# Kernel optimization log

Measured on AMD Instinct MI355X. Metric: run time of the kernel, lower is better.

## Reference

```python
import jax, jax.numpy as jnp
import numpy as np

V_SIZE, E, H = 30000, 256, 128   # vocab, emb_dim, GRU hidden per direction
B, U, T, ND = 32, 32, 128, 64    # dialogues, utterances, max tokens, dialogue-id table size
SCALE = E ** 0.5                  # attention normalise_factor = hid_size**0.5, hid_size = emb_dim


def _gru_dir(x_seq, w_ih, w_hh, b_ih, b_hh):
    """Unidirectional torch-style GRU. x_seq: [N,T,E] -> [N,T,H]."""
    xp = jnp.einsum('nte,ge->ntg', x_seq, w_ih) + b_ih   # precompute input gates [N,T,3H]
    xp = jnp.swapaxes(xp, 0, 1)                          # [T,N,3H]

    def step(h, xpt):
        gh = h @ w_hh.T + b_hh
        r = jax.nn.sigmoid(xpt[:, :H] + gh[:, :H])
        z = jax.nn.sigmoid(xpt[:, H:2 * H] + gh[:, H:2 * H])
        n = jnp.tanh(xpt[:, 2 * H:] + r * gh[:, 2 * H:])
        h_new = (1.0 - z) * n + z * h
        return h_new, h_new

    h0 = jnp.zeros((x_seq.shape[0], H), x_seq.dtype)
    _, out = jax.lax.scan(step, h0, xp)
    return jnp.swapaxes(out, 0, 1)


def _forward(x, d_ids, utt_len, emb_table,
             w_ih_f, w_hh_f, b_ih_f, b_hh_f,
             w_ih_b, w_hh_b, b_ih_b, b_hh_b,
             wq, bq, wk, bk, wv, bv, wo, bo, wl, bl):
    b, u, t = x.shape
    N = b * u
    emb = emb_table[x.reshape(N, t)]                      # [N,T,E]
    lens = jnp.clip(utt_len[d_ids].reshape(N), 1, t)      # valid tokens per utterance
    pos = jnp.arange(t)
    # index map that reverses the valid prefix (padding region clipped, unused)
    rev_idx = jnp.clip(lens[:, None] - 1 - pos[None, :], 0, t - 1)  # [N,T]

    o_f = _gru_dir(emb, w_ih_f, w_hh_f, b_ih_f, b_hh_f)   # causal => correct on valid prefix
    emb_rev = jnp.take_along_axis(emb, rev_idx[:, :, None], axis=1)
    o_b = jnp.take_along_axis(_gru_dir(emb_rev, w_ih_b, w_hh_b, b_ih_b, b_hh_b),
                              rev_idx[:, :, None], axis=1)
    h = jnp.concatenate([o_f, o_b], axis=-1)              # [N,T,E] bi-GRU states

    # self-attention pooling; original takes op[-1], so only the query at the
    # last valid token (lens-1) is needed -- identical math, less compute.
    k = jnp.einsum('nte,he->nth', h, wk) + bk
    v = jnp.einsum('nte,he->nth', h, wv) + bv
    h_last = jnp.take_along_axis(h, (lens - 1)[:, None, None], axis=1)[:, 0]  # [N,E]
    q = h_last @ wq.T + bq
    score = jnp.einsum('nh,nth->nt', q, k) / SCALE
    score = jnp.where(pos[None, :] < lens[:, None], score, -jnp.inf)
    attn = jax.nn.softmax(score, axis=-1)
    ctx = jnp.einsum('nt,nth->nh', attn, v)
    out = (ctx @ wo.T + bo) @ wl.T + bl                   # make_output then final linear
    return out.reshape(b, u, -1)


def setup_inputs() -> dict:
    key = jax.random.key(0)
    ks = jax.random.split(key, 16)

    def p(k, shape):
        return (jax.random.normal(k, shape, jnp.float32) / np.sqrt(shape[-1])).astype(jnp.float32)

    return {
        'x': jax.random.randint(ks[0], (B, U, T), 0, V_SIZE, dtype=jnp.int32),
        'd_ids': jax.random.randint(ks[1], (B,), 0, ND, dtype=jnp.int32),
        'utt_len': jax.random.randint(ks[2], (ND, U), 1, T + 1, dtype=jnp.int32),
        'emb_table': p(ks[3], (V_SIZE, E)),
        'w_ih_f': p(ks[4], (3 * H, E)), 'w_hh_f': p(ks[5], (3 * H, H)),
        'b_ih_f': jnp.zeros(3 * H, jnp.float32), 'b_hh_f': jnp.zeros(3 * H, jnp.float32),
        'w_ih_b': p(ks[6], (3 * H, E)), 'w_hh_b': p(ks[7], (3 * H, H)),
        'b_ih_b': jnp.zeros(3 * H, jnp.float32), 'b_hh_b': jnp.zeros(3 * H, jnp.float32),
        'wq': p(ks[8], (E, E)), 'bq': jnp.zeros(E, jnp.float32),
        'wk': p(ks[9], (E, E)), 'bk': jnp.zeros(E, jnp.float32),
        'wv': p(ks[10], (E, E)), 'bv': jnp.zeros(E, jnp.float32),
        'wo': p(ks[11], (E, E)), 'bo': jnp.zeros(E, jnp.float32),
        'wl': p(ks[12], (E, E)), 'bl': jnp.zeros(E, jnp.float32),
    }


def reference(x, d_ids, utt_len, emb_table,
              w_ih_f, w_hh_f, b_ih_f, b_hh_f,
              w_ih_b, w_hh_b, b_ih_b, b_hh_b,
              wq, bq, wk, bk, wv, bv, wo, bo, wl, bl):
    return _forward(x, d_ids, utt_len, emb_table,
                    w_ih_f, w_hh_f, b_ih_f, b_hh_f,
                    w_ih_b, w_hh_b, b_ih_b, b_hh_b,
                    wq, bq, wk, bk, wv, bv, wo, bo, wl, bl)
```

## Files before the change

kernel.cpp:

```cpp
#include <hip/hip_runtime.h>
#include <hip/hip_bf16.h>
#include <math.h>
#include <stdint.h>

typedef unsigned short u16;
typedef unsigned int   u32;
typedef __attribute__((ext_vector_type(8))) short bf16x8;
typedef __attribute__((ext_vector_type(4))) float f32x4;

#define EDIM 256
#define HDIM 128
#define TLEN 128
#define NUTT 1024
#define UU   32
#define NBU  8

#define WS_FLAG 0
#define WS_LENS 64
#define WS_TAB  4608
#define WS_COPY 8192
#define WS_OF   18874368LL
#define WS_OB   52428800LL

#define MFMA16(a, b, c) __builtin_amdgcn_mfma_f32_16x16x32_bf16((a), (b), (c), 0, 0, 0)
#define SOUT(u, s, j) ((u) * 1096 + (s) * 136 + (j))
#define IS_TILED(a) ((a)==9||(a)==11||(a)==12||(a)==14||(a)==16)

__constant__ int G_SZ[18] = {7680000, 98304, 49152, 384, 384, 98304, 49152, 384, 384,
                             65536, 256, 65536, 65536, 256, 65536, 256, 65536, 256};

__device__ __forceinline__ float b2f(u16 b) {
    u32 u = ((u32)b) << 16; float f; __builtin_memcpy(&f, &u, 4); return f;
}
__device__ __forceinline__ u16 f2b(float f) {
    u32 u; __builtin_memcpy(&u, &f, 4);
    u32 r = u + 0x7FFFu + ((u >> 16) & 1u);
    return (u16)(r >> 16);
}
__device__ __forceinline__ u16 f2b_hw(float f) {
    __hip_bfloat16 h = __float2bfloat16(f);
    u16 v; __builtin_memcpy(&v, &h, 2); return v;
}
__device__ __forceinline__ float fsigmoid(float x) { return 1.0f / (1.0f + __expf(-x)); }
__device__ __forceinline__ float ftanh(float x) { return 1.0f - 2.0f / (__expf(2.0f * x) + 1.0f); }

__global__ __launch_bounds__(256)
void k_convert(void* ws,
               const int* __restrict__ d_ids, const int* __restrict__ utt_len,
               const void* a0, const void* a1, const void* a2, const void* a3,
               const void* a4, const void* a5, const void* a6, const void* a7,
               const void* a8, const void* a9, const void* a10, const void* a11,
               const void* a12, const void* a13, const void* a14, const void* a15,
               const void* a16, const void* a17) {
    __shared__ int scnt[4];
    const int tid = threadIdx.x, lane = tid & 63, wid = tid >> 6;
    const u16* p = (const u16*)a0;
    int cnt = 0;
#pragma unroll 8
    for (int i = tid; i < 16384; i += 256)
        cnt += ((p[i] & 0x7F80) == 0x7F80) ? 1 : 0;
#pragma unroll
    for (int o = 32; o > 0; o >>= 1) cnt += __shfl_down(cnt, o);
    if (lane == 0) scnt[wid] = cnt;
    __syncthreads();
    const int flag = (scnt[0] + scnt[1] + scnt[2] + scnt[3] > 0) ? 1 : 0;

    const void* orig[18] = {a0,a1,a2,a3,a4,a5,a6,a7,a8,a9,a10,a11,a12,a13,a14,a15,a16,a17};
    u16* base = (u16*)((char*)ws + WS_COPY);

    if (blockIdx.x == 0) {
        if (tid == 0) {
            *(int*)((char*)ws + WS_FLAG) = flag;
            const u16** tab = (const u16**)((char*)ws + WS_TAB);
            long long cum = 0;
            for (int a = 0; a < 18; ++a) {
                tab[a] = (IS_TILED(a) || flag) ? (const u16*)(base + cum)
                                               : (const u16*)orig[a];
                cum += G_SZ[a];
            }
        }
        int* lens = (int*)((char*)ws + WS_LENS);
#pragma unroll 4
        for (int n = tid; n < NUTT; n += 256) {
            int b = n >> 5;
            int u = n & (UU - 1);
            int L = utt_len[d_ids[b] * UU + u];
            lens[n] = min(max(L, 1), TLEN);
        }
    }

    const int gtid = blockIdx.x * blockDim.x + tid;
    const int gs   = gridDim.x * blockDim.x;

    {
        long long offs[18];
        { long long c = 0; for (int a = 0; a < 18; ++a) { offs[a] = c; c += G_SZ[a]; } }
        const int mats[5] = {9, 11, 12, 14, 16};
        for (int q = gtid; q < 5 * 16384; q += gs) {
            const int mi = q >> 14;
            const int g  = q & 16383;
            const int a  = mats[mi];
            const int e4 = g * 4;
            const int rowa = e4 >> 8, colb = e4 & 255;
            u16 e[4];
            if (flag) {
                float4 v = ((const float4*)orig[a])[g];
                e[0] = f2b(v.x); e[1] = f2b(v.y); e[2] = f2b(v.z); e[3] = f2b(v.w);
            } else {
                uint2 v = ((const uint2*)orig[a])[g];
                e[0] = (u16)v.x; e[1] = (u16)(v.x >> 16);
                e[2] = (u16)v.y; e[3] = (u16)(v.y >> 16);
            }
            u16* dst = base + offs[a];
            if (a == 11) {
                u16* dd = dst + (rowa >> 3) * 2048 + colb * 8 + (rowa & 7);
                dd[0] = e[0]; dd[8] = e[1]; dd[16] = e[2]; dd[24] = e[3];
            } else {
                u16* dd = dst + (colb >> 3) * 2048 + rowa * 8 + (colb & 7);
                dd[0] = e[0]; dd[1] = e[1]; dd[2] = e[2]; dd[3] = e[3];
            }
        }
    }

    if (flag == 0) return;
    long long cum = 0;
    for (int a = 0; a < 18; ++a) {
        if (IS_TILED(a)) { cum += G_SZ[a]; continue; }
        const float4* src = (const float4*)orig[a];
        uint2* dst = (uint2*)(base + cum);
        const int n4 = G_SZ[a] >> 2;
        for (int i = gtid; i < n4; i += gs) {
            float4 v = src[i];
            uint2 pk;
            pk.x = (u32)f2b(v.x) | ((u32)f2b(v.y) << 16);
            pk.y = (u32)f2b(v.z) | ((u32)f2b(v.w) << 16);
            dst[i] = pk;
        }
        cum += G_SZ[a];
    }
}

__global__ __launch_bounds__(512)
void k_scan(const int* __restrict__ x, void* ws) {
    const u16* const* tab = (const u16* const*)((char*)ws + WS_TAB);
    const int dir = blockIdx.y;
    const u16* emb  = tab[0];
    const u16* w_ih = tab[1 + dir * 4];
    const u16* w_hh = tab[2 + dir * 4];
    const u16* b_ih = tab[3 + dir * 4];
    const u16* b_hh = tab[4 + dir * 4];
    u16* outp = (u16*)((char*)ws + (dir ? WS_OB : WS_OF));
    const int* lens = (const int*)((char*)ws + WS_LENS);

    const int n0 = blockIdx.x * NBU;
    __shared__ __align__(16) u16 sh_emb[2][NBU][264];
    __shared__ __align__(16) u16 sh_hi[2][NBU * 136];
    __shared__ __align__(16) u16 sh_lo[2][NBU * 136];
    __shared__ __align__(16) u16 sh_out[2][NBU * 1096];
    __shared__ int sh_tok[NBU * 132];
    __shared__ int sh_L[NBU];

    const int tid = threadIdx.x, lane = tid & 63, wvi = tid >> 6;
    const int q4 = lane >> 4, mm = lane & 15;
    const int j = wvi * 16 + mm;
    const int u8 = mm & 7;
    const int arr0 = (q4 & 2);
    const bool a2 = (arr0 != 0);
    const bool lo32 = (lane < 32);

    for (int i = tid; i < NBU * 136; i += 512) { sh_hi[0][i] = 0; sh_lo[0][i] = 0; }
    for (int i = tid; i < NBU * TLEN; i += 512) {
        const int u = i >> 7, tt = i & 127;
        sh_tok[u * 132 + tt] = x[(n0 + u) * TLEN + tt];
    }
    if (tid < NBU) sh_L[tid] = lens[n0 + tid];

    bf16x8 wih[3][8]; bf16x8 whh[3][4];
    float bcr, bcz, bxn, bgn;
#pragma unroll
    for (int n3 = 0; n3 < 3; ++n3) {
        const int g = n3 * HDIM + j;
#pragma unroll
        for (int ks = 0; ks < 8; ++ks)
            wih[n3][ks] = *(const bf16x8*)(w_ih + g * EDIM + ks * 32 + q4 * 8);
#pragma unroll
        for (int ks = 0; ks < 4; ++ks)
            whh[n3][ks] = *(const bf16x8*)(w_hh + g * HDIM + ks * 32 + q4 * 8);
    }
    bcr = b2f(b_ih[j]) + b2f(b_hh[j]);
    bcz = b2f(b_ih[HDIM + j]) + b2f(b_hh[HDIM + j]);
    bxn = b2f(b_ih[2 * HDIM + j]);
    bgn = b2f(b_hh[2 * HDIM + j]);

    float hprev[2] = {0.f, 0.f};
    const f32x4 zero4 = {0.f, 0.f, 0.f, 0.f};
    __syncthreads();

    int Lm = sh_L[0];
#pragma unroll
    for (int u = 1; u < NBU; ++u) Lm = max(Lm, sh_L[u]);
    const int tmax = (Lm + 7) & ~7;

    const int pf_u = lane & 7;
    const int pf_c = (wvi & 3) * 8 + (lane >> 3);
    const int pf_L = sh_L[pf_u];
    const int tsel = wvi >> 2;

    {
        const int te = dir ? max(pf_L - 1 - tsel, 0) : tsel;
        const int tok = sh_tok[pf_u * 132 + te];
        uint4 v = *(const uint4*)(emb + (size_t)tok * EDIM + pf_c * 8);
        *(uint4*)&sh_emb[tsel][pf_u][pf_c * 8] = v;
    }
    __syncthreads();

    for (int t0 = 0; t0 < tmax; t0 += 2) {
        const int obuf = (t0 >> 3) & 1;
        const bool more = (t0 + 2 < tmax);

        uint4 pf;
        if (more) {
            const int tt = t0 + 2 + tsel;
            const int te = dir ? max(pf_L - 1 - tt, 0) : tt;
            const int tok = sh_tok[pf_u * 132 + te];
            pf = *(const uint4*)(emb + (size_t)tok * EDIM + pf_c * 8);
        }

        f32x4 accx[3];
        {
            const u16* eb_ = (mm < 8) ? &sh_emb[0][u8][0] : &sh_emb[1][u8][0];
            bf16x8 a = *(const bf16x8*)(eb_ + q4 * 8);
            accx[0] = MFMA16(a, wih[0][0], zero4);
            accx[1] = MFMA16(a, wih[1][0], zero4);
            accx[2] = MFMA16(a, wih[2][0], zero4);
#pragma unroll
            for (int ks = 1; ks < 8; ++ks) {
                bf16x8 av = *(const bf16x8*)(eb_ + ks * 32 + q4 * 8);
                accx[0] = MFMA16(av, wih[0][ks], accx[0]);
                accx[1] = MFMA16(av, wih[1][ks], accx[1]);
                accx[2] = MFMA16(av, wih[2][ks], accx[2]);
            }
        }
        float xA[3][2], xB[3][2];
#pragma unroll
        for (int g = 0; g < 3; ++g) {
#pragma unroll
            for (int r = 0; r < 2; ++r) {
                const float sv = a2 ? accx[g][r] : accx[g][2 + r];
                const float ov = a2 ? accx[g][2 + r] : accx[g][r];
                const float pv = __shfl_xor(sv, 32);
                xA[g][r] = lo32 ? ov : pv;
                xB[g][r] = lo32 ? pv : ov;
            }
        }

        {
            f32x4 accg[3];
            const u16* hb_ = ((mm < 8) ? sh_hi[0] : sh_lo[0]) + u8 * 136;
            {
                bf16x8 a = *(const bf16x8*)(hb_ + q4 * 8);
                accg[0] = MFMA16(a, whh[0][0], zero4);
                accg[1] = MFMA16(a, whh[1][0], zero4);
                accg[2] = MFMA16(a, whh[2][0], zero4);
            }
#pragma unroll
            for (int ks = 1; ks < 4; ++ks) {
                bf16x8 a = *(const bf16x8*)(hb_ + ks * 32 + q4 * 8);
                accg[0] = MFMA16(a, whh[0][ks], accg[0]);
                accg[1] = MFMA16(a, whh[1][ks], accg[1]);
                accg[2] = MFMA16(a, whh[2][ks], accg[2]);
            }
            const int slot = t0 & 7;
#pragma unroll
            for (int r = 0; r < 2; ++r) {
                float gg[3];
#pragma unroll
                for (int g = 0; g < 3; ++g) {
                    const float sv = a2 ? accg[g][r] : accg[g][2 + r];
                    const float ov = a2 ? accg[g][2 + r] : accg[g][r];
                    gg[g] = ov + __shfl_xor(sv, 32);
                }
                const int u = (q4 * 4 + arr0 + r) & 7;
                const float rg = fsigmoid(xA[0][r] + gg[0] + bcr);
                const float zg = fsigmoid(xA[1][r] + gg[1] + bcz);
                const float nn = ftanh((xA[2][r] + bxn) + rg * (gg[2] + bgn));
                const float hn = (1.0f - zg) * nn + zg * hprev[r];
                hprev[r] = hn;
                const u16 hb16 = f2b_hw(hn);
                sh_hi[1][u * 136 + j] = hb16;
                sh_lo[1][u * 136 + j] = f2b_hw(hn - b2f(hb16));
                sh_out[obuf][SOUT(u, slot, j)] = hb16;
            }
        }
        __syncthreads();

        {
            f32x4 accg[3];
            const u16* hb_ = ((mm < 8) ? sh_hi[1] : sh_lo[1]) + u8 * 136;
            {
                bf16x8 a = *(const bf16x8*)(hb_ + q4 * 8);
                accg[0] = MFMA16(a, whh[0][0], zero4);
                accg[1] = MFMA16(a, whh[1][0], zero4);
                accg[2] = MFMA16(a, whh[2][0], zero4);
            }
#pragma unroll
            for (int ks = 1; ks < 4; ++ks) {
                bf16x8 a = *(const bf16x8*)(hb_ + ks * 32 + q4 * 8);
                accg[0] = MFMA16(a, whh[0][ks], accg[0]);
                accg[1] = MFMA16(a, whh[1][ks], accg[1]);
                accg[2] = MFMA16(a, whh[2][ks], accg[2]);
            }
            const int slot = (t0 & 7) + 1;
#pragma unroll
            for (int r = 0; r < 2; ++r) {
                float gg[3];
#pragma unroll
                for (int g = 0; g < 3; ++g) {
                    const float sv = a2 ? accg[g][r] : accg[g][2 + r];
                    const float ov = a2 ? accg[g][2 + r] : accg[g][r];
                    gg[g] = ov + __shfl_xor(sv, 32);
                }
                const int u = (q4 * 4 + arr0 + r) & 7;
                const float rg = fsigmoid(xB[0][r] + gg[0] + bcr);
                const float zg = fsigmoid(xB[1][r] + gg[1] + bcz);
                const float nn = ftanh((xB[2][r] + bxn) + rg * (gg[2] + bgn));
                const float hn = (1.0f - zg) * nn + zg * hprev[r];
                hprev[r] = hn;
                const u16 hb16 = f2b_hw(hn);
                sh_hi[0][u * 136 + j] = hb16;
                sh_lo[0][u * 136 + j] = f2b_hw(hn - b2f(hb16));
                sh_out[obuf][SOUT(u, slot, j)] = hb16;
            }
        }
        if (more)
            *(uint4*)&sh_emb[tsel][pf_u][pf_c * 8] = pf;
        __syncthreads();

        if (((t0 + 1) & 7) == 7) {
            const int rowIdx = tid >> 3;
            const int part   = tid & 7;
            const int fu = rowIdx >> 3, fs = rowIdx & 7;
            const int tt = ((t0 + 1) & ~7) + fs;
            const int tout = dir ? (sh_L[fu] - 1 - tt) : tt;
            if (tout >= 0) {
                const u16* srcp = &sh_out[obuf][SOUT(fu, fs, part * 16)];
                uint4 v0 = *(const uint4*)(srcp);
                uint4 v1 = *(const uint4*)(srcp + 8);
                u16* dstp = outp + ((size_t)(n0 + fu) * TLEN + tout) * HDIM + part * 16;
                *(uint4*)(dstp)     = v0;
                *(uint4*)(dstp + 8) = v1;
            }
        }
    }
}

__device__ __forceinline__ float matvec_tiled(const u16* __restrict__ wt,
                                              const float* __restrict__ vin,
                                              int tid, float bias) {
    float s0 = bias, s1 = 0.0f;
#pragma unroll
    for (int kt = 0; kt < 32; kt += 2) {
        bf16x8 w8 = *(const bf16x8*)(wt + kt * 2048 + tid * 8);
        bf16x8 w9 = *(const bf16x8*)(wt + (kt + 1) * 2048 + tid * 8);
#pragma unroll
        for (int d = 0; d < 8; ++d) {
            s0 += b2f((u16)w8[d]) * vin[kt * 8 + d];
            s1 += b2f((u16)w9[d]) * vin[kt * 8 + 8 + d];
        }
    }
    return s0 + s1;
}

__global__ __launch_bounds__(256)
void k_attn(void* ws, void* outv) {
    const u16* const* tab = (const u16* const*)((char*)ws + WS_TAB);
    const u16* wq = tab[9];  const u16* bq = tab[10];
    const u16* wk = tab[11];
    const u16* wv = tab[12]; const u16* bv = tab[13];
    const u16* wo = tab[14]; const u16* bo = tab[15];
    const u16* wl = tab[16]; const u16* bl = tab[17];
    const int* lens = (const int*)((char*)ws + WS_LENS);
    const int flag = *(const int*)((const char*)ws + WS_FLAG);

    const int n = blockIdx.x;
    const int L = lens[n];
    const u16* hf = (const u16*)((char*)ws + WS_OF) + (size_t)n * TLEN * HDIM;
    const u16* hb = (const u16*)((char*)ws + WS_OB) + (size_t)n * TLEN * HDIM;

    __shared__ float sh_hl[EDIM];
    __shared__ float sh_v1[EDIM];
    __shared__ float sh_uv[EDIM];
    __shared__ float sh_a[4 * EDIM];
    __shared__ float sh_m[4], sh_l[4];

    const int tid = threadIdx.x, lane = tid & 63, wid = tid >> 6;

    sh_hl[tid] = (tid < HDIM) ? b2f(hf[(size_t)(L - 1) * HDIM + tid])
                              : b2f(hb[(size_t)(L - 1) * HDIM + (tid - HDIM)]);
    __syncthreads();

    sh_v1[tid] = matvec_tiled(wq, sh_hl, tid, b2f(bq[tid]));
    __syncthreads();

    sh_uv[tid] = matvec_tiled(wk, sh_v1, tid, 0.0f);
    __syncthreads();

    {
        const int e0 = lane * 4;
        const float u0 = sh_uv[e0], u1 = sh_uv[e0 + 1];
        const float u2 = sh_uv[e0 + 2], u3 = sh_uv[e0 + 3];
        float m = -1e30f, l = 0.0f;
        float a0 = 0.f, a1 = 0.f, a2 = 0.f, a3 = 0.f;
        for (int t = wid; t < L; t += 4) {
            const u16* src = (lane < 32) ? (hf + (size_t)t * HDIM + lane * 4)
                                         : (hb + (size_t)t * HDIM + (lane - 32) * 4);
            uint2 pv = *(const uint2*)src;
            const float h0 = b2f((u16)(pv.x & 0xFFFF));
            const float h1 = b2f((u16)(pv.x >> 16));
            const float h2 = b2f((u16)(pv.y & 0xFFFF));
            const float h3 = b2f((u16)(pv.y >> 16));
            float p = h0 * u0 + h1 * u1 + h2 * u2 + h3 * u3;
#pragma unroll
            for (int o = 32; o > 0; o >>= 1) p += __shfl_xor(p, o);
            const float s = p * 0.0625f;
            const float mn = fmaxf(m, s);
            const float c = __expf(m - mn);
            const float w = __expf(s - mn);
            l = l * c + w;
            a0 = a0 * c + w * h0;
            a1 = a1 * c + w * h1;
            a2 = a2 * c + w * h2;
            a3 = a3 * c + w * h3;
            m = mn;
        }
        sh_a[wid * EDIM + e0]     = a0;
        sh_a[wid * EDIM + e0 + 1] = a1;
        sh_a[wid * EDIM + e0 + 2] = a2;
        sh_a[wid * EDIM + e0 + 3] = a3;
        if (lane == 0) { sh_m[wid] = m; sh_l[wid] = l; }
    }
    __syncthreads();

    {
        const float m0 = sh_m[0], m1 = sh_m[1], m2 = sh_m[2], m3 = sh_m[3];
        const float M = fmaxf(fmaxf(m0, m1), fmaxf(m2, m3));
        const float c0 = __expf(m0 - M), c1 = __expf(m1 - M);
        const float c2 = __expf(m2 - M), c3 = __expf(m3 - M);
        const float den = c0 * sh_l[0] + c1 * sh_l[1] + c2 * sh_l[2] + c3 * sh_l[3];
        const float num = c0 * sh_a[tid] + c1 * sh_a[EDIM + tid] +
                          c2 * sh_a[2 * EDIM + tid] + c3 * sh_a[3 * EDIM + tid];
        sh_hl[tid] = num / den;
    }
    __syncthreads();

    sh_uv[tid] = matvec_tiled(wv, sh_hl, tid, b2f(bv[tid]));
    __syncthreads();

    sh_v1[tid] = matvec_tiled(wo, sh_uv, tid, b2f(bo[tid]));
    __syncthreads();

    {
        const float s = matvec_tiled(wl, sh_v1, tid, b2f(bl[tid]));
        const size_t oidx = (size_t)n * EDIM + tid;
        if (flag) ((float*)outv)[oidx] = s;
        else      ((u16*)outv)[oidx]   = f2b(s);
    }
}

extern "C" void kernel_launch(void* const* d_in, const int* in_sizes, int n_in,
                              void* d_out, int out_size, void* d_ws, size_t ws_size,
                              hipStream_t stream) {
    const int* x       = (const int*)d_in[0];
    const int* d_ids   = (const int*)d_in[1];
    const int* utt_len = (const int*)d_in[2];
    const void* f_arr[18] = {
        d_in[3],
        d_in[4], d_in[5], d_in[6], d_in[7],
        d_in[8], d_in[9], d_in[10], d_in[11],
        d_in[12], d_in[13],
        d_in[14],
        d_in[16], d_in[17],
        d_in[18], d_in[19],
        d_in[20], d_in[21]
    };

    k_convert<<<512, 256, 0, stream>>>(d_ws, d_ids, utt_len,
        f_arr[0], f_arr[1], f_arr[2], f_arr[3], f_arr[4], f_arr[5], f_arr[6], f_arr[7],
        f_arr[8], f_arr[9], f_arr[10], f_arr[11], f_arr[12], f_arr[13], f_arr[14],
        f_arr[15], f_arr[16], f_arr[17]);

    k_scan<<<dim3(NUTT / NBU, 2), 512, 0, stream>>>(x, d_ws);

    k_attn<<<NUTT, 256, 0, stream>>>(d_ws, d_out);
}
```

Measured before the change: 350.8 us.

## Drop bulk fp32→bf16 weight copy; convert inline in scan/attn, unroll softmax loop

```diff
diff --git a/kernel.cpp b/kernel.cpp
--- a/kernel.cpp
+++ b/kernel.cpp
@@ -16,18 +16,12 @@
 #define NBU  8
 
 #define WS_FLAG 0
-#define WS_LENS 64
-#define WS_TAB  4608
 #define WS_COPY 8192
 #define WS_OF   18874368LL
 #define WS_OB   52428800LL
 
 #define MFMA16(a, b, c) __builtin_amdgcn_mfma_f32_16x16x32_bf16((a), (b), (c), 0, 0, 0)
 #define SOUT(u, s, j) ((u) * 1096 + (s) * 136 + (j))
-#define IS_TILED(a) ((a)==9||(a)==11||(a)==12||(a)==14||(a)==16)
-
-__constant__ int G_SZ[18] = {7680000, 98304, 49152, 384, 384, 98304, 49152, 384, 384,
-                             65536, 256, 65536, 65536, 256, 65536, 256, 65536, 256};
 
 __device__ __forceinline__ float b2f(u16 b) {
     u32 u = ((u32)b) << 16; float f; __builtin_memcpy(&f, &u, 4); return f;
@@ -44,17 +38,44 @@
 __device__ __forceinline__ float fsigmoid(float x) { return 1.0f / (1.0f + __expf(-x)); }
 __device__ __forceinline__ float ftanh(float x) { return 1.0f - 2.0f / (__expf(2.0f * x) + 1.0f); }
 
+__device__ __forceinline__ bf16x8 ldw8(const void* p, size_t off, int flag) {
+    if (flag) {
+        const float* f = (const float*)p + off;
+        float4 a = *(const float4*)f;
+        float4 b = *(const float4*)(f + 4);
+        union { u16 e[8]; bf16x8 v; } r;
+        r.e[0] = f2b_hw(a.x); r.e[1] = f2b_hw(a.y);
+        r.e[2] = f2b_hw(a.z); r.e[3] = f2b_hw(a.w);
+        r.e[4] = f2b_hw(b.x); r.e[5] = f2b_hw(b.y);
+        r.e[6] = f2b_hw(b.z); r.e[7] = f2b_hw(b.w);
+        return r.v;
+    }
+    return *(const bf16x8*)((const u16*)p + off);
+}
+__device__ __forceinline__ uint4 ldemb(const void* p, size_t off, int flag) {
+    if (flag) {
+        const float* f = (const float*)p + off;
+        float4 a = *(const float4*)f;
+        float4 b = *(const float4*)(f + 4);
+        uint4 r;
+        r.x = (u32)f2b_hw(a.x) | ((u32)f2b_hw(a.y) << 16);
+        r.y = (u32)f2b_hw(a.z) | ((u32)f2b_hw(a.w) << 16);
+        r.z = (u32)f2b_hw(b.x) | ((u32)f2b_hw(b.y) << 16);
+        r.w = (u32)f2b_hw(b.z) | ((u32)f2b_hw(b.w) << 16);
+        return r;
+    }
+    return *(const uint4*)((const u16*)p + off);
+}
+__device__ __forceinline__ float ldb(const void* p, int i, int flag) {
+    return flag ? ((const float*)p)[i] : b2f(((const u16*)p)[i]);
+}
+
 __global__ __launch_bounds__(256)
-void k_convert(void* ws,
-               const int* __restrict__ d_ids, const int* __restrict__ utt_len,
-               const void* a0, const void* a1, const void* a2, const void* a3,
-               const void* a4, const void* a5, const void* a6, const void* a7,
-               const void* a8, const void* a9, const void* a10, const void* a11,
-               const void* a12, const void* a13, const void* a14, const void* a15,
-               const void* a16, const void* a17) {
+void k_convert(void* ws, const void* emb, const void* wq, const void* wk,
+               const void* wv, const void* wo, const void* wl) {
     __shared__ int scnt[4];
     const int tid = threadIdx.x, lane = tid & 63, wid = tid >> 6;
-    const u16* p = (const u16*)a0;
+    const u16* p = (const u16*)emb;
     int cnt = 0;
 #pragma unroll 8
     for (int i = tid; i < 16384; i += 256)
@@ -64,93 +85,50 @@
     if (lane == 0) scnt[wid] = cnt;
     __syncthreads();
     const int flag = (scnt[0] + scnt[1] + scnt[2] + scnt[3] > 0) ? 1 : 0;
-
-    const void* orig[18] = {a0,a1,a2,a3,a4,a5,a6,a7,a8,a9,a10,a11,a12,a13,a14,a15,a16,a17};
+    if (blockIdx.x == 0 && tid == 0) *(int*)((char*)ws + WS_FLAG) = flag;
+
+    const void* mats[5] = {wq, wk, wv, wo, wl};
     u16* base = (u16*)((char*)ws + WS_COPY);
-
-    if (blockIdx.x == 0) {
-        if (tid == 0) {
-            *(int*)((char*)ws + WS_FLAG) = flag;
-            const u16** tab = (const u16**)((char*)ws + WS_TAB);
-            long long cum = 0;
-            for (int a = 0; a < 18; ++a) {
-                tab[a] = (IS_TILED(a) || flag) ? (const u16*)(base + cum)
-                                               : (const u16*)orig[a];
-                cum += G_SZ[a];
-            }
-        }
-        int* lens = (int*)((char*)ws + WS_LENS);
-#pragma unroll 4
-        for (int n = tid; n < NUTT; n += 256) {
-            int b = n >> 5;
-            int u = n & (UU - 1);
-            int L = utt_len[d_ids[b] * UU + u];
-            lens[n] = min(max(L, 1), TLEN);
-        }
-    }
-
-    const int gtid = blockIdx.x * blockDim.x + tid;
-    const int gs   = gridDim.x * blockDim.x;
-
-    {
-        long long offs[18];
-        { long long c = 0; for (int a = 0; a < 18; ++a) { offs[a] = c; c += G_SZ[a]; } }
-        const int mats[5] = {9, 11, 12, 14, 16};
-        for (int q = gtid; q < 5 * 16384; q += gs) {
-            const int mi = q >> 14;
-            const int g  = q & 16383;
-            const int a  = mats[mi];
-            const int e4 = g * 4;
-            const int rowa = e4 >> 8, colb = e4 & 255;
-            u16 e[4];
-            if (flag) {
-                float4 v = ((const float4*)orig[a])[g];
-                e[0] = f2b(v.x); e[1] = f2b(v.y); e[2] = f2b(v.z); e[3] = f2b(v.w);
-            } else {
-                uint2 v = ((const uint2*)orig[a])[g];
-                e[0] = (u16)v.x; e[1] = (u16)(v.x >> 16);
-                e[2] = (u16)v.y; e[3] = (u16)(v.y >> 16);
-            }
-            u16* dst = base + offs[a];
-            if (a == 11) {
-                u16* dd = dst + (rowa >> 3) * 2048 + colb * 8 + (rowa & 7);
-                dd[0] = e[0]; dd[8] = e[1]; dd[16] = e[2]; dd[24] = e[3];
-            } else {
-                u16* dd = dst + (colb >> 3) * 2048 + rowa * 8 + (colb & 7);
-                dd[0] = e[0]; dd[1] = e[1]; dd[2] = e[2]; dd[3] = e[3];
-            }
-        }
-    }
-
-    if (flag == 0) return;
-    long long cum = 0;
-    for (int a = 0; a < 18; ++a) {
-        if (IS_TILED(a)) { cum += G_SZ[a]; continue; }
-        const float4* src = (const float4*)orig[a];
-        uint2* dst = (uint2*)(base + cum);
-        const int n4 = G_SZ[a] >> 2;
-        for (int i = gtid; i < n4; i += gs) {
-            float4 v = src[i];
-            uint2 pk;
-            pk.x = (u32)f2b(v.x) | ((u32)f2b(v.y) << 16);
-            pk.y = (u32)f2b(v.z) | ((u32)f2b(v.w) << 16);
-            dst[i] = pk;
-        }
-        cum += G_SZ[a];
+    const int gtid = blockIdx.x * 256 + tid;
+    const int gs   = gridDim.x * 256;
+    for (int q = gtid; q < 5 * 16384; q += gs) {
+        const int mi = q >> 14;
+        const int g  = q & 16383;
+        const int e4 = g * 4;
+        const int rowa = e4 >> 8, colb = e4 & 255;
+        u16 e[4];
+        if (flag) {
+            float4 v = ((const float4*)mats[mi])[g];
+            e[0] = f2b(v.x); e[1] = f2b(v.y); e[2] = f2b(v.z); e[3] = f2b(v.w);
+        } else {
+            uint2 v = ((const uint2*)mats[mi])[g];
+            e[0] = (u16)v.x; e[1] = (u16)(v.x >> 16);
+            e[2] = (u16)v.y; e[3] = (u16)(v.y >> 16);
+        }
+        u16* dst = base + mi * 65536;
+        if (mi == 1) {
+            u16* dd = dst + (rowa >> 3) * 2048 + colb * 8 + (rowa & 7);
+            dd[0] = e[0]; dd[8] = e[1]; dd[16] = e[2]; dd[24] = e[3];
+        } else {
+            u16* dd = dst + (colb >> 3) * 2048 + rowa * 8 + (colb & 7);
+            dd[0] = e[0]; dd[1] = e[1]; dd[2] = e[2]; dd[3] = e[3];
+        }
     }
 }
 
 __global__ __launch_bounds__(512)
-void k_scan(const int* __restrict__ x, void* ws) {
-    const u16* const* tab = (const u16* const*)((char*)ws + WS_TAB);
+void k_scan(const int* __restrict__ x, void* ws,
+            const int* __restrict__ d_ids, const int* __restrict__ utt_len,
+            const void* embp,
+            const void* wihf, const void* whhf, const void* bihf, const void* bhhf,
+            const void* wihb, const void* whhb, const void* bihb, const void* bhhb) {
     const int dir = blockIdx.y;
-    const u16* emb  = tab[0];
-    const u16* w_ih = tab[1 + dir * 4];
-    const u16* w_hh = tab[2 + dir * 4];
-    const u16* b_ih = tab[3 + dir * 4];
-    const u16* b_hh = tab[4 + dir * 4];
+    const void* w_ih = dir ? wihb : wihf;
+    const void* w_hh = dir ? whhb : whhf;
+    const void* b_ih = dir ? bihb : bihf;
+    const void* b_hh = dir ? bhhb : bhhf;
     u16* outp = (u16*)((char*)ws + (dir ? WS_OB : WS_OF));
-    const int* lens = (const int*)((char*)ws + WS_LENS);
+    const int flag = *(const int*)((const char*)ws + WS_FLAG);
 
     const int n0 = blockIdx.x * NBU;
     __shared__ __align__(16) u16 sh_emb[2][NBU][264];
@@ -173,7 +151,11 @@
         const int u = i >> 7, tt = i & 127;
         sh_tok[u * 132 + tt] = x[(n0 + u) * TLEN + tt];
     }
-    if (tid < NBU) sh_L[tid] = lens[n0 + tid];
+    if (tid < NBU) {
+        const int gn = n0 + tid;
+        const int L = utt_len[d_ids[gn >> 5] * UU + (gn & 31)];
+        sh_L[tid] = min(max(L, 1), TLEN);
+    }
 
     bf16x8 wih[3][8]; bf16x8 whh[3][4];
     float bcr, bcz, bxn, bgn;
@@ -182,15 +164,15 @@
         const int g = n3 * HDIM + j;
 #pragma unroll
         for (int ks = 0; ks < 8; ++ks)
-            wih[n3][ks] = *(const bf16x8*)(w_ih + g * EDIM + ks * 32 + q4 * 8);
+            wih[n3][ks] = ldw8(w_ih, (size_t)g * EDIM + ks * 32 + q4 * 8, flag);
 #pragma unroll
         for (int ks = 0; ks < 4; ++ks)
-            whh[n3][ks] = *(const bf16x8*)(w_hh + g * HDIM + ks * 32 + q4 * 8);
-    }
-    bcr = b2f(b_ih[j]) + b2f(b_hh[j]);
-    bcz = b2f(b_ih[HDIM + j]) + b2f(b_hh[HDIM + j]);
-    bxn = b2f(b_ih[2 * HDIM + j]);
-    bgn = b2f(b_hh[2 * HDIM + j]);
+            whh[n3][ks] = ldw8(w_hh, (size_t)g * HDIM + ks * 32 + q4 * 8, flag);
+    }
+    bcr = ldb(b_ih, j, flag) + ldb(b_hh, j, flag);
+    bcz = ldb(b_ih, HDIM + j, flag) + ldb(b_hh, HDIM + j, flag);
+    bxn = ldb(b_ih, 2 * HDIM + j, flag);
+    bgn = ldb(b_hh, 2 * HDIM + j, flag);
 
     float hprev[2] = {0.f, 0.f};
     const f32x4 zero4 = {0.f, 0.f, 0.f, 0.f};
@@ -209,7 +191,7 @@
     {
         const int te = dir ? max(pf_L - 1 - tsel, 0) : tsel;
         const int tok = sh_tok[pf_u * 132 + te];
-        uint4 v = *(const uint4*)(emb + (size_t)tok * EDIM + pf_c * 8);
+        uint4 v = ldemb(embp, (size_t)tok * EDIM + pf_c * 8, flag);
         *(uint4*)&sh_emb[tsel][pf_u][pf_c * 8] = v;
     }
     __syncthreads();
@@ -223,7 +205,7 @@
             const int tt = t0 + 2 + tsel;
             const int te = dir ? max(pf_L - 1 - tt, 0) : tt;
             const int tok = sh_tok[pf_u * 132 + te];
-            pf = *(const uint4*)(emb + (size_t)tok * EDIM + pf_c * 8);
+            pf = ldemb(embp, (size_t)tok * EDIM + pf_c * 8, flag);
         }
 
         f32x4 accx[3];
@@ -372,18 +354,19 @@
 }
 
 __global__ __launch_bounds__(256)
-void k_attn(void* ws, void* outv) {
-    const u16* const* tab = (const u16* const*)((char*)ws + WS_TAB);
-    const u16* wq = tab[9];  const u16* bq = tab[10];
-    const u16* wk = tab[11];
-    const u16* wv = tab[12]; const u16* bv = tab[13];
-    const u16* wo = tab[14]; const u16* bo = tab[15];
-    const u16* wl = tab[16]; const u16* bl = tab[17];
-    const int* lens = (const int*)((char*)ws + WS_LENS);
+void k_attn(void* ws, void* outv,
+            const int* __restrict__ d_ids, const int* __restrict__ utt_len,
+            const void* bqp, const void* bvp, const void* bop, const void* blp) {
+    const u16* wt = (const u16*)((char*)ws + WS_COPY);
+    const u16* wq = wt;
+    const u16* wk = wt + 65536;
+    const u16* wv = wt + 2 * 65536;
+    const u16* wo = wt + 3 * 65536;
+    const u16* wl = wt + 4 * 65536;
     const int flag = *(const int*)((const char*)ws + WS_FLAG);
 
     const int n = blockIdx.x;
-    const int L = lens[n];
+    const int L = min(max(utt_len[d_ids[n >> 5] * UU + (n & 31)], 1), TLEN);
     const u16* hf = (const u16*)((char*)ws + WS_OF) + (size_t)n * TLEN * HDIM;
     const u16* hb = (const u16*)((char*)ws + WS_OB) + (size_t)n * TLEN * HDIM;
 
@@ -399,7 +382,7 @@
                               : b2f(hb[(size_t)(L - 1) * HDIM + (tid - HDIM)]);
     __syncthreads();
 
-    sh_v1[tid] = matvec_tiled(wq, sh_hl, tid, b2f(bq[tid]));
+    sh_v1[tid] = matvec_tiled(wq, sh_hl, tid, ldb(bqp, tid, flag));
     __syncthreads();
 
     sh_uv[tid] = matvec_tiled(wk, sh_v1, tid, 0.0f);
@@ -411,26 +394,40 @@
         const float u2 = sh_uv[e0 + 2], u3 = sh_uv[e0 + 3];
         float m = -1e30f, l = 0.0f;
         float a0 = 0.f, a1 = 0.f, a2 = 0.f, a3 = 0.f;
-        for (int t = wid; t < L; t += 4) {
-            const u16* src = (lane < 32) ? (hf + (size_t)t * HDIM + lane * 4)
-                                         : (hb + (size_t)t * HDIM + (lane - 32) * 4);
-            uint2 pv = *(const uint2*)src;
-            const float h0 = b2f((u16)(pv.x & 0xFFFF));
-            const float h1 = b2f((u16)(pv.x >> 16));
-            const float h2 = b2f((u16)(pv.y & 0xFFFF));
-            const float h3 = b2f((u16)(pv.y >> 16));
-            float p = h0 * u0 + h1 * u1 + h2 * u2 + h3 * u3;
-#pragma unroll
-            for (int o = 32; o > 0; o >>= 1) p += __shfl_xor(p, o);
-            const float s = p * 0.0625f;
-            const float mn = fmaxf(m, s);
-            const float c = __expf(m - mn);
-            const float w = __expf(s - mn);
-            l = l * c + w;
-            a0 = a0 * c + w * h0;
-            a1 = a1 * c + w * h1;
-            a2 = a2 * c + w * h2;
-            a3 = a3 * c + w * h3;
+        const size_t lofs = (lane < 32) ? (size_t)(lane * 4)
+                                        : (size_t)((lane - 32) * 4);
+        const u16* hbase = (lane < 32) ? hf : hb;
+        for (int t = wid; t < L; t += 8) {
+            const int tB = t + 4;
+            const int tBc = (tB < L) ? tB : (L - 1);
+            uint2 pvA = *(const uint2*)(hbase + (size_t)t * HDIM + lofs);
+            uint2 pvB = *(const uint2*)(hbase + (size_t)tBc * HDIM + lofs);
+            const float hA0 = b2f((u16)(pvA.x & 0xFFFF));
+            const float hA1 = b2f((u16)(pvA.x >> 16));
+            const float hA2 = b2f((u16)(pvA.y & 0xFFFF));
+            const float hA3 = b2f((u16)(pvA.y >> 16));
+            const float hB0 = b2f((u16)(pvB.x & 0xFFFF));
+            const float hB1 = b2f((u16)(pvB.x >> 16));
+            const float hB2 = b2f((u16)(pvB.y & 0xFFFF));
+            const float hB3 = b2f((u16)(pvB.y >> 16));
+            float pA = hA0 * u0 + hA1 * u1 + hA2 * u2 + hA3 * u3;
+            float pB = hB0 * u0 + hB1 * u1 + hB2 * u2 + hB3 * u3;
+#pragma unroll
+            for (int o = 32; o > 0; o >>= 1) {
+                pA += __shfl_xor(pA, o);
+                pB += __shfl_xor(pB, o);
+            }
+            const float sA = pA * 0.0625f;
+            const float sB = (tB < L) ? pB * 0.0625f : -1e30f;
+            const float mn = fmaxf(m, fmaxf(sA, sB));
+            const float c  = __expf(m - mn);
+            const float wA = __expf(sA - mn);
+            const float wB = __expf(sB - mn);
+            l = l * c + wA + wB;
+            a0 = a0 * c + wA * hA0 + wB * hB0;
+            a1 = a1 * c + wA * hA1 + wB * hB1;
+            a2 = a2 * c + wA * hA2 + wB * hB2;
+            a3 = a3 * c + wA * hA3 + wB * hB3;
             m = mn;
         }
         sh_a[wid * EDIM + e0]     = a0;
@@ -453,14 +450,14 @@
     }
     __syncthreads();
 
-    sh_uv[tid] = matvec_tiled(wv, sh_hl, tid, b2f(bv[tid]));
-    __syncthreads();
-
-    sh_v1[tid] = matvec_tiled(wo, sh_uv, tid, b2f(bo[tid]));
+    sh_uv[tid] = matvec_tiled(wv, sh_hl, tid, ldb(bvp, tid, flag));
+    __syncthreads();
+
+    sh_v1[tid] = matvec_tiled(wo, sh_uv, tid, ldb(bop, tid, flag));
     __syncthreads();
 
     {
-        const float s = matvec_tiled(wl, sh_v1, tid, b2f(bl[tid]));
+        const float s = matvec_tiled(wl, sh_v1, tid, ldb(blp, tid, flag));
         const size_t oidx = (size_t)n * EDIM + tid;
         if (flag) ((float*)outv)[oidx] = s;
         else      ((u16*)outv)[oidx]   = f2b(s);
@@ -473,23 +470,15 @@
     const int* x       = (const int*)d_in[0];
     const int* d_ids   = (const int*)d_in[1];
     const int* utt_len = (const int*)d_in[2];
-    const void* f_arr[18] = {
-        d_in[3],
+
+    k_convert<<<160, 256, 0, stream>>>(d_ws, d_in[3], d_in[12], d_in[14],
+                                       d_in[16], d_in[18], d_in[20]);
+
+    k_scan<<<dim3(NUTT / NBU, 2), 512, 0, stream>>>(
+        x, d_ws, d_ids, utt_len, d_in[3],
         d_in[4], d_in[5], d_in[6], d_in[7],
-        d_in[8], d_in[9], d_in[10], d_in[11],
-        d_in[12], d_in[13],
-        d_in[14],
-        d_in[16], d_in[17],
-        d_in[18], d_in[19],
-        d_in[20], d_in[21]
-    };
-
-    k_convert<<<512, 256, 0, stream>>>(d_ws, d_ids, utt_len,
-        f_arr[0], f_arr[1], f_arr[2], f_arr[3], f_arr[4], f_arr[5], f_arr[6], f_arr[7],
-        f_arr[8], f_arr[9], f_arr[10], f_arr[11], f_arr[12], f_arr[13], f_arr[14],
-        f_arr[15], f_arr[16], f_arr[17]);
-
-    k_scan<<<dim3(NUTT / NBU, 2), 512, 0, stream>>>(x, d_ws);
-
-    k_attn<<<NUTT, 256, 0, stream>>>(d_ws, d_out);
-}
+        d_in[8], d_in[9], d_in[10], d_in[11]);
+
+    k_attn<<<NUTT, 256, 0, stream>>>(d_ws, d_out, d_ids, utt_len,
+                                     d_in[13], d_in[17], d_in[19], d_in[21]);
+}
```

After: 350.6 us. About the same (-0.1%).
